# Kernel optimization log

Hardware: AMD Instinct MI355X
Metric: run time of the kernel (lower is better)

## Reference

```python
import jax, jax.numpy as jnp
import numpy as np

INPUTS_SIZE = 128
HIDDEN_SIZE = 256
BATCH = 65536


def hard_sigmoid(x):
    # torch.nn.Hardsigmoid: relu6(x + 3) / 6
    return jnp.clip(x / 6.0 + 0.5, 0.0, 1.0)


def hard_tanh(x):
    return jnp.clip(x, -1.0, 1.0)


def setup_inputs() -> dict:
    key = jax.random.key(0)
    ks = jax.random.split(key, 8)
    cat = INPUTS_SIZE + HIDDEN_SIZE
    s = 1.0 / np.sqrt(cat)
    return {
        "inputs": jax.random.normal(ks[0], (BATCH, INPUTS_SIZE), dtype=jnp.float32),
        "h_prev": jax.random.normal(ks[1], (BATCH, HIDDEN_SIZE), dtype=jnp.float32),
        "W_z": jax.random.uniform(ks[2], (HIDDEN_SIZE, cat), jnp.float32, -s, s),
        "b_z": jax.random.uniform(ks[3], (HIDDEN_SIZE,), jnp.float32, -s, s),
        "W_r": jax.random.uniform(ks[4], (HIDDEN_SIZE, cat), jnp.float32, -s, s),
        "b_r": jax.random.uniform(ks[5], (HIDDEN_SIZE,), jnp.float32, -s, s),
        "W_h": jax.random.uniform(ks[6], (HIDDEN_SIZE, cat), jnp.float32, -s, s),
        "b_h": jax.random.uniform(ks[7], (HIDDEN_SIZE,), jnp.float32, -s, s),
    }


def reference(inputs, h_prev, W_z, b_z, W_r, b_r, W_h, b_h):
    # concat(inputs, h_prev) along feature dim: [B, I+H]
    ih = jnp.concatenate([inputs, h_prev], axis=-1)
    # update gate z and reset gate r (HardSigmoid activations)
    z = hard_sigmoid(ih @ W_z.T + b_z)  # [B, H]
    r = hard_sigmoid(ih @ W_r.T + b_r)  # [B, H]
    # candidate: concat(inputs, r * h_prev) -> linear -> HardTanh
    irh = jnp.concatenate([inputs, r * h_prev], axis=-1)
    h_tilde = hard_tanh(irh @ W_h.T + b_h)  # [B, H]
    # h_next = z * h_prev + (1 - z) * h_tilde
    h_next = z * h_prev + (1.0 - z) * h_tilde
    return h_next
```

## Files before the change

### kernel.cpp

```cpp
#include <hip/hip_runtime.h>


#define BATCH 65536
#define ISZ   128
#define HSZ   256
#define CAT   384
#define BM    64
#define NT    512
#define ROWB  768
#define ACT_B (BM * ROWB)
#define CH_B  16384

using half8   = __attribute__((ext_vector_type(8))) _Float16;
using floatx4 = __attribute__((ext_vector_type(4))) float;

typedef unsigned int u32;
typedef __attribute__((address_space(1))) const u32 gu32;
typedef __attribute__((address_space(3))) u32 lu32;

__device__ __forceinline__ void gload16(const void* g, void* l) {
    __builtin_amdgcn_global_load_lds((gu32*)g, (lu32*)l, 16, 0, 0);
}

#define BAR()      __builtin_amdgcn_s_barrier()
#define SCHED0()   __builtin_amdgcn_sched_barrier(0)
#define WAIT_VM2() asm volatile("s_waitcnt vmcnt(2)" ::: "memory")
#define WAIT_VM0() asm volatile("s_waitcnt vmcnt(0)" ::: "memory")
#define WAIT_LG0() asm volatile("s_waitcnt lgkmcnt(0)" ::: "memory")
#define MFMA       __builtin_amdgcn_mfma_f32_16x16x32_f16

__device__ __forceinline__ float hsig(float x) {
    return fminf(fmaxf(x * (1.0f / 6.0f) + 0.5f, 0.0f), 1.0f);
}
__device__ __forceinline__ float htanh(float x) {
    return fminf(fmaxf(x, -1.0f), 1.0f);
}
__device__ __forceinline__ half8 cvt8(float4 v0, float4 v1) {
    half8 h;
    h[0] = (_Float16)v0.x; h[1] = (_Float16)v0.y;
    h[2] = (_Float16)v0.z; h[3] = (_Float16)v0.w;
    h[4] = (_Float16)v1.x; h[5] = (_Float16)v1.y;
    h[6] = (_Float16)v1.z; h[7] = (_Float16)v1.w;
    return h;
}

__global__ __launch_bounds__(256) void prep_weights(
    const float* __restrict__ Wz, const float* __restrict__ Wr,
    const float* __restrict__ Wh, _Float16* __restrict__ ws)
{
    const int m = blockIdx.y;
    const float* src = (m == 0) ? Wz : (m == 1) ? Wr : Wh;
    _Float16* dst = ws + (size_t)m * (HSZ * CAT);
    const int base = (blockIdx.x * 256 + threadIdx.x) * 8;
    float4 v0 = *(const float4*)(src + base);
    float4 v1 = *(const float4*)(src + base + 4);
    *(half8*)(dst + base) = cvt8(v0, v1);
}

__device__ __forceinline__ void issue_chunk(const _Float16* __restrict__ wf,
                                            unsigned char* wbuf, int c,
                                            int w, int lane) {
    const _Float16* src = (c < 24) ? (wf + (c & 1) * (HSZ * CAT))
                                   : (wf + 2 * (HSZ * CAT));
    const int kk = (c < 24) ? (c >> 1) : (c - 24);
    unsigned char* dst = wbuf + (c & 1) * CH_B;
    #pragma unroll
    for (int ii = 0; ii < 2; ++ii) {
        const int i = w * 2 + ii;
        const int n = i * 16 + (lane >> 2);
        const int ss = (lane & 3) ^ ((n >> 1) & 3);
        gload16(src + n * CAT + kk * 32 + ss * 8, dst + i * 1024);
    }
}

__device__ __forceinline__ half8 wread(const unsigned char* buf, int n, int lk) {
    return *(const half8*)(buf + n * 64 + ((lk ^ ((n >> 1) & 3)) << 4));
}

__global__ __launch_bounds__(NT, 4) void gru_kernel(
    const float* __restrict__ x, const float* __restrict__ h_prev,
    const float* __restrict__ b_z, const float* __restrict__ b_r,
    const float* __restrict__ b_h, const _Float16* __restrict__ wf,
    float* __restrict__ out)
{
    __shared__ __align__(16) unsigned char lds[ACT_B + 2 * CH_B];
    unsigned char* const act  = lds;
    unsigned char* const wbuf = lds + ACT_B;

    const int t    = threadIdx.x;
    const int lane = t & 63;
    const int w    = t >> 6;
    const int mg   = w >> 2;
    const int ng   = w & 3;
    const int lr   = lane & 15;
    const int lk   = lane >> 4;
    const int row0 = blockIdx.x * BM;

    issue_chunk(wf, wbuf, 0, w, lane);
    issue_chunk(wf, wbuf, 1, w, lane);

    float bhv[4];
    floatx4 accz[2][4], accr[2][4];
    #pragma unroll
    for (int j = 0; j < 4; ++j) {
        const int col = ng * 64 + j * 16 + lr;
        const float vz = b_z[col];
        const float vr = b_r[col];
        bhv[j] = b_h[col];
        floatx4 tz = {vz, vz, vz, vz};
        floatx4 tr = {vr, vr, vr, vr};
        accz[0][j] = tz; accz[1][j] = tz;
        accr[0][j] = tr; accr[1][j] = tr;
    }

    for (int c = t; c < BM * 16; c += NT) {
        int row = c >> 4, kc = c & 15;
        const float* g = x + (size_t)(row0 + row) * ISZ + kc * 8;
        float4 v0 = *(const float4*)g;
        float4 v1 = *(const float4*)(g + 4);
        *(half8*)(act + row * ROWB + ((kc * 16) ^ ((row & 7) << 4))) = cvt8(v0, v1);
    }
    for (int c = t; c < BM * 32; c += NT) {
        int row = c >> 5, kc = c & 31;
        const float* g = h_prev + (size_t)(row0 + row) * HSZ + kc * 8;
        float4 v0 = *(const float4*)g;
        float4 v1 = *(const float4*)(g + 4);
        *(half8*)(act + row * ROWB + ((256 + kc * 16) ^ ((row & 7) << 4))) = cvt8(v0, v1);
    }
    WAIT_VM0(); WAIT_LG0(); SCHED0();
    BAR();

    const int rowA = mg * 32 + lr;
    const int asw  = (rowA & 7) << 4;

    half8 a0, a1;

    #pragma unroll 1
    for (int kk = 0; kk < 12; ++kk) {
        WAIT_VM2(); SCHED0(); BAR();
        a0 = *(const half8*)(act + rowA * ROWB        + ((kk * 64 + lk * 16) ^ asw));
        a1 = *(const half8*)(act + (rowA + 16) * ROWB + ((kk * 64 + lk * 16) ^ asw));
        __builtin_amdgcn_s_setprio(1);
        #pragma unroll
        for (int j = 0; j < 4; ++j) {
            half8 bf = wread(wbuf, ng * 64 + j * 16 + lr, lk);
            accz[0][j] = MFMA(a0, bf, accz[0][j], 0, 0, 0);
            accz[1][j] = MFMA(a1, bf, accz[1][j], 0, 0, 0);
        }
        __builtin_amdgcn_s_setprio(0);
        WAIT_LG0(); SCHED0(); BAR();
        issue_chunk(wf, wbuf, 2 * kk + 2, w, lane);
        WAIT_VM2(); SCHED0(); BAR();
        __builtin_amdgcn_s_setprio(1);
        #pragma unroll
        for (int j = 0; j < 4; ++j) {
            half8 bf = wread(wbuf + CH_B, ng * 64 + j * 16 + lr, lk);
            accr[0][j] = MFMA(a0, bf, accr[0][j], 0, 0, 0);
            accr[1][j] = MFMA(a1, bf, accr[1][j], 0, 0, 0);
        }
        __builtin_amdgcn_s_setprio(0);
        WAIT_LG0(); SCHED0(); BAR();
        issue_chunk(wf, wbuf, 2 * kk + 3, w, lane);
    }

    #pragma unroll
    for (int f = 0; f < 2; ++f) {
        #pragma unroll
        for (int j = 0; j < 4; ++j) {
            #pragma unroll
            for (int q = 0; q < 4; ++q) {
                const int row = mg * 32 + f * 16 + lk * 4 + q;
                const int col = ng * 64 + j * 16 + lr;
                accz[f][j][q] = hsig(accz[f][j][q]);
                float rr = hsig(accr[f][j][q]);
                _Float16* hp = (_Float16*)(act + row * ROWB +
                                           ((256 + col * 2) ^ ((row & 7) << 4)));
                float hv = (float)hp[0];
                hp[0] = (_Float16)(rr * hv);
            }
        }
    }
    WAIT_LG0();

    floatx4 acch[2][4];
    #pragma unroll
    for (int j = 0; j < 4; ++j) {
        floatx4 th = {bhv[j], bhv[j], bhv[j], bhv[j]};
        acch[0][j] = th; acch[1][j] = th;
    }
    #pragma unroll 1
    for (int kk = 0; kk < 12; ++kk) {
        if (kk < 11) { WAIT_VM2(); } else { WAIT_VM0(); }
        SCHED0(); BAR();
        const unsigned char* buf = wbuf + (kk & 1) * CH_B;
        a0 = *(const half8*)(act + rowA * ROWB        + ((kk * 64 + lk * 16) ^ asw));
        a1 = *(const half8*)(act + (rowA + 16) * ROWB + ((kk * 64 + lk * 16) ^ asw));
        __builtin_amdgcn_s_setprio(1);
        #pragma unroll
        for (int j = 0; j < 4; ++j) {
            half8 bf = wread(buf, ng * 64 + j * 16 + lr, lk);
            acch[0][j] = MFMA(a0, bf, acch[0][j], 0, 0, 0);
            acch[1][j] = MFMA(a1, bf, acch[1][j], 0, 0, 0);
        }
        __builtin_amdgcn_s_setprio(0);
        WAIT_LG0(); SCHED0(); BAR();
        if (kk < 10) issue_chunk(wf, wbuf, 26 + kk, w, lane);
    }

    #pragma unroll
    for (int f = 0; f < 2; ++f) {
        #pragma unroll
        for (int j = 0; j < 4; ++j) {
            #pragma unroll
            for (int q = 0; q < 4; ++q) {
                const int row = mg * 32 + f * 16 + lk * 4 + q;
                const int col = ng * 64 + j * 16 + lr;
                float ht = htanh(acch[f][j][q]);
                float zz = accz[f][j][q];
                float hv = h_prev[(size_t)(row0 + row) * HSZ + col];
                out[(size_t)(row0 + row) * HSZ + col] = zz * hv + (1.0f - zz) * ht;
            }
        }
    }
}

extern "C" void kernel_launch(void* const* d_in, const int* in_sizes, int n_in,
                              void* d_out, int out_size, void* d_ws, size_t ws_size,
                              hipStream_t stream) {
    const float* x  = (const float*)d_in[0];
    const float* h  = (const float*)d_in[1];
    const float* Wz = (const float*)d_in[2];
    const float* bz = (const float*)d_in[3];
    const float* Wr = (const float*)d_in[4];
    const float* br = (const float*)d_in[5];
    const float* Wh = (const float*)d_in[6];
    const float* bh = (const float*)d_in[7];
    _Float16* wf = (_Float16*)d_ws;

    prep_weights<<<dim3(48, 3), 256, 0, stream>>>(Wz, Wr, Wh, wf);
    gru_kernel<<<dim3(BATCH / BM), NT, 0, stream>>>(
        x, h, bz, br, bh, wf, (float*)d_out);
}
```

Baseline: 198.5 us.

## Halve block to four waves each computing full 64-row tiles per column slice

Cuts the block from eight waves to four. Each wave now covers all 64 rows for a 64-column slice, so every B-fragment read from LDS feeds four MFMAs instead of two, and each wave issues twice as many weight loads per chunk. The r*h_prev product now reads h_prev in fp32 from global memory instead of the fp16 copy in LDS, which slightly changes rounding. The cost is twice the accumulator registers per thread (launch bounds lowered to 2 blocks) and fewer waves to hide latency.

Result: slower. 205.7 us (+3.6%).

```diff
diff --git a/kernel.cpp b/kernel.cpp
--- a/kernel.cpp
+++ b/kernel.cpp
@@ -6,7 +6,7 @@
 #define HSZ   256
 #define CAT   384
 #define BM    64
-#define NT    512
+#define NT    256
 #define ROWB  768
 #define ACT_B (BM * ROWB)
 #define CH_B  16384
@@ -24,7 +24,7 @@
 
 #define BAR()      __builtin_amdgcn_s_barrier()
 #define SCHED0()   __builtin_amdgcn_sched_barrier(0)
-#define WAIT_VM2() asm volatile("s_waitcnt vmcnt(2)" ::: "memory")
+#define WAIT_VM4() asm volatile("s_waitcnt vmcnt(4)" ::: "memory")
 #define WAIT_VM0() asm volatile("s_waitcnt vmcnt(0)" ::: "memory")
 #define WAIT_LG0() asm volatile("s_waitcnt lgkmcnt(0)" ::: "memory")
 #define MFMA       __builtin_amdgcn_mfma_f32_16x16x32_f16
@@ -65,8 +65,8 @@
     const int kk = (c < 24) ? (c >> 1) : (c - 24);
     unsigned char* dst = wbuf + (c & 1) * CH_B;
     #pragma unroll
-    for (int ii = 0; ii < 2; ++ii) {
-        const int i = w * 2 + ii;
+    for (int ii = 0; ii < 4; ++ii) {
+        const int i = w * 4 + ii;
         const int n = i * 16 + (lane >> 2);
         const int ss = (lane & 3) ^ ((n >> 1) & 3);
         gload16(src + n * CAT + kk * 32 + ss * 8, dst + i * 1024);
@@ -77,7 +77,7 @@
     return *(const half8*)(buf + n * 64 + ((lk ^ ((n >> 1) & 3)) << 4));
 }
 
-__global__ __launch_bounds__(NT, 4) void gru_kernel(
+__global__ __launch_bounds__(NT, 2) void gru_kernel(
     const float* __restrict__ x, const float* __restrict__ h_prev,
     const float* __restrict__ b_z, const float* __restrict__ b_r,
     const float* __restrict__ b_h, const _Float16* __restrict__ wf,
@@ -90,8 +90,6 @@
     const int t    = threadIdx.x;
     const int lane = t & 63;
     const int w    = t >> 6;
-    const int mg   = w >> 2;
-    const int ng   = w & 3;
     const int lr   = lane & 15;
     const int lk   = lane >> 4;
     const int row0 = blockIdx.x * BM;
@@ -100,17 +98,17 @@
     issue_chunk(wf, wbuf, 1, w, lane);
 
     float bhv[4];
-    floatx4 accz[2][4], accr[2][4];
+    floatx4 accz[4][4], accr[4][4];
     #pragma unroll
     for (int j = 0; j < 4; ++j) {
-        const int col = ng * 64 + j * 16 + lr;
+        const int col = w * 64 + j * 16 + lr;
         const float vz = b_z[col];
         const float vr = b_r[col];
         bhv[j] = b_h[col];
         floatx4 tz = {vz, vz, vz, vz};
         floatx4 tr = {vr, vr, vr, vr};
-        accz[0][j] = tz; accz[1][j] = tz;
-        accr[0][j] = tr; accr[1][j] = tr;
+        #pragma unroll
+        for (int f = 0; f < 4; ++f) { accz[f][j] = tz; accr[f][j] = tr; }
     }
 
     for (int c = t; c < BM * 16; c += NT) {
@@ -130,33 +128,36 @@
     WAIT_VM0(); WAIT_LG0(); SCHED0();
     BAR();
 
-    const int rowA = mg * 32 + lr;
-    const int asw  = (rowA & 7) << 4;
-
-    half8 a0, a1;
+    half8 a[4];
 
     #pragma unroll 1
     for (int kk = 0; kk < 12; ++kk) {
-        WAIT_VM2(); SCHED0(); BAR();
-        a0 = *(const half8*)(act + rowA * ROWB        + ((kk * 64 + lk * 16) ^ asw));
-        a1 = *(const half8*)(act + (rowA + 16) * ROWB + ((kk * 64 + lk * 16) ^ asw));
+        WAIT_VM4(); SCHED0(); BAR();
+        #pragma unroll
+        for (int f = 0; f < 4; ++f) {
+            const int row = f * 16 + lr;
+            a[f] = *(const half8*)(act + row * ROWB +
+                                   ((kk * 64 + lk * 16) ^ ((row & 7) << 4)));
+        }
         __builtin_amdgcn_s_setprio(1);
         #pragma unroll
         for (int j = 0; j < 4; ++j) {
-            half8 bf = wread(wbuf, ng * 64 + j * 16 + lr, lk);
-            accz[0][j] = MFMA(a0, bf, accz[0][j], 0, 0, 0);
-            accz[1][j] = MFMA(a1, bf, accz[1][j], 0, 0, 0);
+            half8 bf = wread(wbuf, w * 64 + j * 16 + lr, lk);
+            #pragma unroll
+            for (int f = 0; f < 4; ++f)
+                accz[f][j] = MFMA(a[f], bf, accz[f][j], 0, 0, 0);
         }
         __builtin_amdgcn_s_setprio(0);
         WAIT_LG0(); SCHED0(); BAR();
         issue_chunk(wf, wbuf, 2 * kk + 2, w, lane);
-        WAIT_VM2(); SCHED0(); BAR();
+        WAIT_VM4(); SCHED0(); BAR();
         __builtin_amdgcn_s_setprio(1);
         #pragma unroll
         for (int j = 0; j < 4; ++j) {
-            half8 bf = wread(wbuf + CH_B, ng * 64 + j * 16 + lr, lk);
-            accr[0][j] = MFMA(a0, bf, accr[0][j], 0, 0, 0);
-            accr[1][j] = MFMA(a1, bf, accr[1][j], 0, 0, 0);
+            half8 bf = wread(wbuf + CH_B, w * 64 + j * 16 + lr, lk);
+            #pragma unroll
+            for (int f = 0; f < 4; ++f)
+                accr[f][j] = MFMA(a[f], bf, accr[f][j], 0, 0, 0);
         }
         __builtin_amdgcn_s_setprio(0);
         WAIT_LG0(); SCHED0(); BAR();
@@ -164,43 +165,49 @@
     }
 
     #pragma unroll
-    for (int f = 0; f < 2; ++f) {
+    for (int f = 0; f < 4; ++f) {
         #pragma unroll
         for (int j = 0; j < 4; ++j) {
             #pragma unroll
             for (int q = 0; q < 4; ++q) {
-                const int row = mg * 32 + f * 16 + lk * 4 + q;
-                const int col = ng * 64 + j * 16 + lr;
+                const int row = f * 16 + lk * 4 + q;
+                const int col = w * 64 + j * 16 + lr;
                 accz[f][j][q] = hsig(accz[f][j][q]);
                 float rr = hsig(accr[f][j][q]);
-                _Float16* hp = (_Float16*)(act + row * ROWB +
-                                           ((256 + col * 2) ^ ((row & 7) << 4)));
-                float hv = (float)hp[0];
-                hp[0] = (_Float16)(rr * hv);
+                float hv = h_prev[(size_t)(row0 + row) * HSZ + col];
+                *(_Float16*)(act + row * ROWB +
+                             ((256 + col * 2) ^ ((row & 7) << 4))) =
+                    (_Float16)(rr * hv);
             }
         }
     }
     WAIT_LG0();
 
-    floatx4 acch[2][4];
+    floatx4 acch[4][4];
     #pragma unroll
     for (int j = 0; j < 4; ++j) {
         floatx4 th = {bhv[j], bhv[j], bhv[j], bhv[j]};
-        acch[0][j] = th; acch[1][j] = th;
+        #pragma unroll
+        for (int f = 0; f < 4; ++f) acch[f][j] = th;
     }
     #pragma unroll 1
     for (int kk = 0; kk < 12; ++kk) {
-        if (kk < 11) { WAIT_VM2(); } else { WAIT_VM0(); }
+        if (kk < 11) { WAIT_VM4(); } else { WAIT_VM0(); }
         SCHED0(); BAR();
         const unsigned char* buf = wbuf + (kk & 1) * CH_B;
-        a0 = *(const half8*)(act + rowA * ROWB        + ((kk * 64 + lk * 16) ^ asw));
-        a1 = *(const half8*)(act + (rowA + 16) * ROWB + ((kk * 64 + lk * 16) ^ asw));
+        #pragma unroll
+        for (int f = 0; f < 4; ++f) {
+            const int row = f * 16 + lr;
+            a[f] = *(const half8*)(act + row * ROWB +
+                                   ((kk * 64 + lk * 16) ^ ((row & 7) << 4)));
+        }
         __builtin_amdgcn_s_setprio(1);
         #pragma unroll
         for (int j = 0; j < 4; ++j) {
-            half8 bf = wread(buf, ng * 64 + j * 16 + lr, lk);
-            acch[0][j] = MFMA(a0, bf, acch[0][j], 0, 0, 0);
-            acch[1][j] = MFMA(a1, bf, acch[1][j], 0, 0, 0);
+            half8 bf = wread(buf, w * 64 + j * 16 + lr, lk);
+            #pragma unroll
+            for (int f = 0; f < 4; ++f)
+                acch[f][j] = MFMA(a[f], bf, acch[f][j], 0, 0, 0);
         }
         __builtin_amdgcn_s_setprio(0);
         WAIT_LG0(); SCHED0(); BAR();
@@ -208,13 +215,13 @@
     }
 
     #pragma unroll
-    for (int f = 0; f < 2; ++f) {
+    for (int f = 0; f < 4; ++f) {
         #pragma unroll
         for (int j = 0; j < 4; ++j) {
             #pragma unroll
             for (int q = 0; q < 4; ++q) {
-                const int row = mg * 32 + f * 16 + lk * 4 + q;
-                const int col = ng * 64 + j * 16 + lr;
+                const int row = f * 16 + lk * 4 + q;
+                const int col = w * 64 + j * 16 + lr;
                 float ht = htanh(acch[f][j][q]);
                 float zz = accz[f][j][q];
                 float hv = h_prev[(size_t)(row0 + row) * HSZ + col];
```

## Triple-buffer weight chunks and stream x directly from global into registers

Applied to the files above, without the earlier changes.

The weight staging ring grows from two to three LDS buffers. This lets each chunk prefetch be issued before the MFMAs on the current buffer, and removes one barrier per half-iteration. The x portion of the activation tile is no longer staged in LDS. Each wave loads its x fragment from global memory, converts it to fp16 at use during the first four K steps, and re-reads it in the candidate pass. This trades LDS footprint and x staging for extra global loads, and the vmcnt-based waits now have to account for the mixed x and weight loads in flight.

New measurement: 215.5 us. 1.09x slower.

```diff
diff --git a/kernel.cpp b/kernel.cpp
--- a/kernel.cpp
+++ b/kernel.cpp
@@ -7,8 +7,8 @@
 #define CAT   384
 #define BM    64
 #define NT    512
-#define ROWB  768
-#define ACT_B (BM * ROWB)
+#define HROWB 512
+#define ACT_B (BM * HROWB)
 #define CH_B  16384
 
 using half8   = __attribute__((ext_vector_type(8))) _Float16;
@@ -63,7 +63,7 @@
     const _Float16* src = (c < 24) ? (wf + (c & 1) * (HSZ * CAT))
                                    : (wf + 2 * (HSZ * CAT));
     const int kk = (c < 24) ? (c >> 1) : (c - 24);
-    unsigned char* dst = wbuf + (c & 1) * CH_B;
+    unsigned char* dst = wbuf + (c % 3) * CH_B;
     #pragma unroll
     for (int ii = 0; ii < 2; ++ii) {
         const int i = w * 2 + ii;
@@ -83,7 +83,7 @@
     const float* __restrict__ b_h, const _Float16* __restrict__ wf,
     float* __restrict__ out)
 {
-    __shared__ __align__(16) unsigned char lds[ACT_B + 2 * CH_B];
+    __shared__ __align__(16) unsigned char lds[ACT_B + 3 * CH_B];
     unsigned char* const act  = lds;
     unsigned char* const wbuf = lds + ACT_B;
 
@@ -113,56 +113,62 @@
         accr[0][j] = tr; accr[1][j] = tr;
     }
 
-    for (int c = t; c < BM * 16; c += NT) {
-        int row = c >> 4, kc = c & 15;
-        const float* g = x + (size_t)(row0 + row) * ISZ + kc * 8;
-        float4 v0 = *(const float4*)g;
-        float4 v1 = *(const float4*)(g + 4);
-        *(half8*)(act + row * ROWB + ((kc * 16) ^ ((row & 7) << 4))) = cvt8(v0, v1);
-    }
     for (int c = t; c < BM * 32; c += NT) {
         int row = c >> 5, kc = c & 31;
         const float* g = h_prev + (size_t)(row0 + row) * HSZ + kc * 8;
         float4 v0 = *(const float4*)g;
         float4 v1 = *(const float4*)(g + 4);
-        *(half8*)(act + row * ROWB + ((256 + kc * 16) ^ ((row & 7) << 4))) = cvt8(v0, v1);
-    }
-    WAIT_VM0(); WAIT_LG0(); SCHED0();
+        *(half8*)(act + row * HROWB + ((kc * 16) ^ ((row & 7) << 4))) = cvt8(v0, v1);
+    }
+    WAIT_LG0(); SCHED0();
     BAR();
 
     const int rowA = mg * 32 + lr;
-    const int asw  = (rowA & 7) << 4;
+    const int asw  = (lr & 7) << 4;
 
     half8 a0, a1;
 
     #pragma unroll 1
     for (int kk = 0; kk < 12; ++kk) {
         WAIT_VM2(); SCHED0(); BAR();
-        a0 = *(const half8*)(act + rowA * ROWB        + ((kk * 64 + lk * 16) ^ asw));
-        a1 = *(const half8*)(act + (rowA + 16) * ROWB + ((kk * 64 + lk * 16) ^ asw));
+        if (kk < 4) {
+            const float* g0 = x + (size_t)(row0 + rowA) * ISZ + kk * 32 + lk * 8;
+            float4 u0 = *(const float4*)g0;
+            float4 u1 = *(const float4*)(g0 + 4);
+            float4 u2 = *(const float4*)(g0 + 16 * ISZ);
+            float4 u3 = *(const float4*)(g0 + 16 * ISZ + 4);
+            issue_chunk(wf, wbuf, 2 * kk + 2, w, lane);
+            a0 = cvt8(u0, u1);
+            a1 = cvt8(u2, u3);
+        } else {
+            issue_chunk(wf, wbuf, 2 * kk + 2, w, lane);
+            const int off = (kk - 4) * 64 + lk * 16;
+            a0 = *(const half8*)(act + rowA * HROWB        + (off ^ asw));
+            a1 = *(const half8*)(act + (rowA + 16) * HROWB + (off ^ asw));
+        }
+        const unsigned char* bz = wbuf + ((2 * kk) % 3) * CH_B;
         __builtin_amdgcn_s_setprio(1);
         #pragma unroll
         for (int j = 0; j < 4; ++j) {
-            half8 bf = wread(wbuf, ng * 64 + j * 16 + lr, lk);
+            half8 bf = wread(bz, ng * 64 + j * 16 + lr, lk);
             accz[0][j] = MFMA(a0, bf, accz[0][j], 0, 0, 0);
             accz[1][j] = MFMA(a1, bf, accz[1][j], 0, 0, 0);
         }
         __builtin_amdgcn_s_setprio(0);
-        WAIT_LG0(); SCHED0(); BAR();
-        issue_chunk(wf, wbuf, 2 * kk + 2, w, lane);
         WAIT_VM2(); SCHED0(); BAR();
+        issue_chunk(wf, wbuf, 2 * kk + 3, w, lane);
+        const unsigned char* brb = wbuf + ((2 * kk + 1) % 3) * CH_B;
         __builtin_amdgcn_s_setprio(1);
         #pragma unroll
         for (int j = 0; j < 4; ++j) {
-            half8 bf = wread(wbuf + CH_B, ng * 64 + j * 16 + lr, lk);
+            half8 bf = wread(brb, ng * 64 + j * 16 + lr, lk);
             accr[0][j] = MFMA(a0, bf, accr[0][j], 0, 0, 0);
             accr[1][j] = MFMA(a1, bf, accr[1][j], 0, 0, 0);
         }
         __builtin_amdgcn_s_setprio(0);
-        WAIT_LG0(); SCHED0(); BAR();
-        issue_chunk(wf, wbuf, 2 * kk + 3, w, lane);
-    }
-
+    }
+
+    BAR();
     #pragma unroll
     for (int f = 0; f < 2; ++f) {
         #pragma unroll
@@ -173,14 +179,14 @@
                 const int col = ng * 64 + j * 16 + lr;
                 accz[f][j][q] = hsig(accz[f][j][q]);
                 float rr = hsig(accr[f][j][q]);
-                _Float16* hp = (_Float16*)(act + row * ROWB +
-                                           ((256 + col * 2) ^ ((row & 7) << 4)));
+                _Float16* hp = (_Float16*)(act + row * HROWB +
+                                           ((col * 2) ^ ((row & 7) << 4)));
                 float hv = (float)hp[0];
                 hp[0] = (_Float16)(rr * hv);
             }
         }
     }
-    WAIT_LG0();
+    WAIT_LG0(); SCHED0();
 
     floatx4 acch[2][4];
     #pragma unroll
@@ -192,19 +198,30 @@
     for (int kk = 0; kk < 12; ++kk) {
         if (kk < 11) { WAIT_VM2(); } else { WAIT_VM0(); }
         SCHED0(); BAR();
-        const unsigned char* buf = wbuf + (kk & 1) * CH_B;
-        a0 = *(const half8*)(act + rowA * ROWB        + ((kk * 64 + lk * 16) ^ asw));
-        a1 = *(const half8*)(act + (rowA + 16) * ROWB + ((kk * 64 + lk * 16) ^ asw));
+        if (kk < 4) {
+            const float* g0 = x + (size_t)(row0 + rowA) * ISZ + kk * 32 + lk * 8;
+            float4 u0 = *(const float4*)g0;
+            float4 u1 = *(const float4*)(g0 + 4);
+            float4 u2 = *(const float4*)(g0 + 16 * ISZ);
+            float4 u3 = *(const float4*)(g0 + 16 * ISZ + 4);
+            if (kk < 10) issue_chunk(wf, wbuf, 26 + kk, w, lane);
+            a0 = cvt8(u0, u1);
+            a1 = cvt8(u2, u3);
+        } else {
+            if (kk < 10) issue_chunk(wf, wbuf, 26 + kk, w, lane);
+            const int off = (kk - 4) * 64 + lk * 16;
+            a0 = *(const half8*)(act + rowA * HROWB        + (off ^ asw));
+            a1 = *(const half8*)(act + (rowA + 16) * HROWB + (off ^ asw));
+        }
+        const unsigned char* bh_ = wbuf + ((24 + kk) % 3) * CH_B;
         __builtin_amdgcn_s_setprio(1);
         #pragma unroll
         for (int j = 0; j < 4; ++j) {
-            half8 bf = wread(buf, ng * 64 + j * 16 + lr, lk);
+            half8 bf = wread(bh_, ng * 64 + j * 16 + lr, lk);
             acch[0][j] = MFMA(a0, bf, acch[0][j], 0, 0, 0);
             acch[1][j] = MFMA(a1, bf, acch[1][j], 0, 0, 0);
         }
         __builtin_amdgcn_s_setprio(0);
-        WAIT_LG0(); SCHED0(); BAR();
-        if (kk < 10) issue_chunk(wf, wbuf, 26 + kk, w, lane);
     }
 
     #pragma unroll
```

## Load weight fragments directly from global memory in MFMA-ready layout, dropping LDS staging

Applied to the files above, without the earlier changes.

Weights are now converted once into a fragment-ordered fp16 layout, so each lane reads its B operand for the MFMA straight from global memory (L2/cache) and the weights no longer pass through LDS. This removes the double-buffered LDS weight staging and most of the per-step barriers. With less LDS per block the occupancy hint is raised from 4 to 6. In exchange every wave re-reads the weights from cache with no reuse across waves, so the MFMA inputs now carry global-load latency.

Result: slower. 325.9 us (+64.2%).

```diff
diff --git a/kernel.cpp b/kernel.cpp
--- a/kernel.cpp
+++ b/kernel.cpp
@@ -9,25 +9,12 @@
 #define NT    512
 #define ROWB  768
 #define ACT_B (BM * ROWB)
-#define CH_B  16384
+#define MSTR  196608
 
 using half8   = __attribute__((ext_vector_type(8))) _Float16;
 using floatx4 = __attribute__((ext_vector_type(4))) float;
 
-typedef unsigned int u32;
-typedef __attribute__((address_space(1))) const u32 gu32;
-typedef __attribute__((address_space(3))) u32 lu32;
-
-__device__ __forceinline__ void gload16(const void* g, void* l) {
-    __builtin_amdgcn_global_load_lds((gu32*)g, (lu32*)l, 16, 0, 0);
-}
-
-#define BAR()      __builtin_amdgcn_s_barrier()
-#define SCHED0()   __builtin_amdgcn_sched_barrier(0)
-#define WAIT_VM2() asm volatile("s_waitcnt vmcnt(2)" ::: "memory")
-#define WAIT_VM0() asm volatile("s_waitcnt vmcnt(0)" ::: "memory")
-#define WAIT_LG0() asm volatile("s_waitcnt lgkmcnt(0)" ::: "memory")
-#define MFMA       __builtin_amdgcn_mfma_f32_16x16x32_f16
+#define MFMA __builtin_amdgcn_mfma_f32_16x16x32_f16
 
 __device__ __forceinline__ float hsig(float x) {
     return fminf(fmaxf(x * (1.0f / 6.0f) + 0.5f, 0.0f), 1.0f);
@@ -46,46 +33,32 @@
 
 __global__ __launch_bounds__(256) void prep_weights(
     const float* __restrict__ Wz, const float* __restrict__ Wr,
-    const float* __restrict__ Wh, _Float16* __restrict__ ws)
+    const float* __restrict__ Wh, unsigned char* __restrict__ ws)
 {
-    const int m = blockIdx.y;
+    const int m  = blockIdx.y;
+    const int kk = blockIdx.x;
     const float* src = (m == 0) ? Wz : (m == 1) ? Wr : Wh;
-    _Float16* dst = ws + (size_t)m * (HSZ * CAT);
-    const int base = (blockIdx.x * 256 + threadIdx.x) * 8;
-    float4 v0 = *(const float4*)(src + base);
-    float4 v1 = *(const float4*)(src + base + 4);
-    *(half8*)(dst + base) = cvt8(v0, v1);
-}
-
-__device__ __forceinline__ void issue_chunk(const _Float16* __restrict__ wf,
-                                            unsigned char* wbuf, int c,
-                                            int w, int lane) {
-    const _Float16* src = (c < 24) ? (wf + (c & 1) * (HSZ * CAT))
-                                   : (wf + 2 * (HSZ * CAT));
-    const int kk = (c < 24) ? (c >> 1) : (c - 24);
-    unsigned char* dst = wbuf + (c & 1) * CH_B;
-    #pragma unroll
-    for (int ii = 0; ii < 2; ++ii) {
-        const int i = w * 2 + ii;
-        const int n = i * 16 + (lane >> 2);
-        const int ss = (lane & 3) ^ ((n >> 1) & 3);
-        gload16(src + n * CAT + kk * 32 + ss * 8, dst + i * 1024);
-    }
-}
-
-__device__ __forceinline__ half8 wread(const unsigned char* buf, int n, int lk) {
-    return *(const half8*)(buf + n * 64 + ((lk ^ ((n >> 1) & 3)) << 4));
-}
-
-__global__ __launch_bounds__(NT, 4) void gru_kernel(
+    const int t = threadIdx.x;
+    const int l = t & 63;
+    #pragma unroll
+    for (int c4 = 0; c4 < 4; ++c4) {
+        const int c   = c4 * 4 + (t >> 6);
+        const int col = c * 16 + (l & 15);
+        const int k0  = kk * 32 + (l >> 4) * 8;
+        float4 v0 = *(const float4*)(src + col * CAT + k0);
+        float4 v1 = *(const float4*)(src + col * CAT + k0 + 4);
+        *(half8*)(ws + (size_t)(m * 192 + kk * 16 + c) * 1024 + l * 16) =
+            cvt8(v0, v1);
+    }
+}
+
+__global__ __launch_bounds__(NT, 6) void gru_kernel(
     const float* __restrict__ x, const float* __restrict__ h_prev,
     const float* __restrict__ b_z, const float* __restrict__ b_r,
-    const float* __restrict__ b_h, const _Float16* __restrict__ wf,
+    const float* __restrict__ b_h, const unsigned char* __restrict__ wsF,
     float* __restrict__ out)
 {
-    __shared__ __align__(16) unsigned char lds[ACT_B + 2 * CH_B];
-    unsigned char* const act  = lds;
-    unsigned char* const wbuf = lds + ACT_B;
+    __shared__ __align__(16) unsigned char act[ACT_B];
 
     const int t    = threadIdx.x;
     const int lane = t & 63;
@@ -96,8 +69,7 @@
     const int lk   = lane >> 4;
     const int row0 = blockIdx.x * BM;
 
-    issue_chunk(wf, wbuf, 0, w, lane);
-    issue_chunk(wf, wbuf, 1, w, lane);
+    const unsigned char* fb = wsF + (size_t)(ng * 4) * 1024 + lane * 16;
 
     float bhv[4];
     floatx4 accz[2][4], accr[2][4];
@@ -127,41 +99,36 @@
         float4 v1 = *(const float4*)(g + 4);
         *(half8*)(act + row * ROWB + ((256 + kc * 16) ^ ((row & 7) << 4))) = cvt8(v0, v1);
     }
-    WAIT_VM0(); WAIT_LG0(); SCHED0();
-    BAR();
+    __syncthreads();
 
     const int rowA = mg * 32 + lr;
-    const int asw  = (rowA & 7) << 4;
-
-    half8 a0, a1;
-
-    #pragma unroll 1
+    const int asw  = (lr & 7) << 4;
+
+    #pragma unroll 2
     for (int kk = 0; kk < 12; ++kk) {
-        WAIT_VM2(); SCHED0(); BAR();
-        a0 = *(const half8*)(act + rowA * ROWB        + ((kk * 64 + lk * 16) ^ asw));
-        a1 = *(const half8*)(act + (rowA + 16) * ROWB + ((kk * 64 + lk * 16) ^ asw));
-        __builtin_amdgcn_s_setprio(1);
-        #pragma unroll
-        for (int j = 0; j < 4; ++j) {
-            half8 bf = wread(wbuf, ng * 64 + j * 16 + lr, lk);
-            accz[0][j] = MFMA(a0, bf, accz[0][j], 0, 0, 0);
-            accz[1][j] = MFMA(a1, bf, accz[1][j], 0, 0, 0);
-        }
-        __builtin_amdgcn_s_setprio(0);
-        WAIT_LG0(); SCHED0(); BAR();
-        issue_chunk(wf, wbuf, 2 * kk + 2, w, lane);
-        WAIT_VM2(); SCHED0(); BAR();
-        __builtin_amdgcn_s_setprio(1);
-        #pragma unroll
-        for (int j = 0; j < 4; ++j) {
-            half8 bf = wread(wbuf + CH_B, ng * 64 + j * 16 + lr, lk);
-            accr[0][j] = MFMA(a0, bf, accr[0][j], 0, 0, 0);
-            accr[1][j] = MFMA(a1, bf, accr[1][j], 0, 0, 0);
-        }
-        __builtin_amdgcn_s_setprio(0);
-        WAIT_LG0(); SCHED0(); BAR();
-        issue_chunk(wf, wbuf, 2 * kk + 3, w, lane);
-    }
+        half8 a0 = *(const half8*)(act + rowA * ROWB +
+                                   ((kk * 64 + lk * 16) ^ asw));
+        half8 a1 = *(const half8*)(act + (rowA + 16) * ROWB +
+                                   ((kk * 64 + lk * 16) ^ asw));
+        const unsigned char* pk = fb + kk * 16384;
+        half8 bz[4], br[4];
+        #pragma unroll
+        for (int j = 0; j < 4; ++j) bz[j] = *(const half8*)(pk + j * 1024);
+        #pragma unroll
+        for (int j = 0; j < 4; ++j) br[j] = *(const half8*)(pk + MSTR + j * 1024);
+        #pragma unroll
+        for (int j = 0; j < 4; ++j) {
+            accz[0][j] = MFMA(a0, bz[j], accz[0][j], 0, 0, 0);
+            accz[1][j] = MFMA(a1, bz[j], accz[1][j], 0, 0, 0);
+        }
+        #pragma unroll
+        for (int j = 0; j < 4; ++j) {
+            accr[0][j] = MFMA(a0, br[j], accr[0][j], 0, 0, 0);
+            accr[1][j] = MFMA(a1, br[j], accr[1][j], 0, 0, 0);
+        }
+    }
+
+    __syncthreads();
 
     #pragma unroll
     for (int f = 0; f < 2; ++f) {
@@ -180,7 +147,7 @@
             }
         }
     }
-    WAIT_LG0();
+    __syncthreads();
 
     floatx4 acch[2][4];
     #pragma unroll
@@ -188,23 +155,21 @@
         floatx4 th = {bhv[j], bhv[j], bhv[j], bhv[j]};
         acch[0][j] = th; acch[1][j] = th;
     }
-    #pragma unroll 1
+    #pragma unroll 2
     for (int kk = 0; kk < 12; ++kk) {
-        if (kk < 11) { WAIT_VM2(); } else { WAIT_VM0(); }
-        SCHED0(); BAR();
-        const unsigned char* buf = wbuf + (kk & 1) * CH_B;
-        a0 = *(const half8*)(act + rowA * ROWB        + ((kk * 64 + lk * 16) ^ asw));
-        a1 = *(const half8*)(act + (rowA + 16) * ROWB + ((kk * 64 + lk * 16) ^ asw));
-        __builtin_amdgcn_s_setprio(1);
-        #pragma unroll
-        for (int j = 0; j < 4; ++j) {
-            half8 bf = wread(buf, ng * 64 + j * 16 + lr, lk);
-            acch[0][j] = MFMA(a0, bf, acch[0][j], 0, 0, 0);
-            acch[1][j] = MFMA(a1, bf, acch[1][j], 0, 0, 0);
-        }
-        __builtin_amdgcn_s_setprio(0);
-        WAIT_LG0(); SCHED0(); BAR();
-        if (kk < 10) issue_chunk(wf, wbuf, 26 + kk, w, lane);
+        half8 a0 = *(const half8*)(act + rowA * ROWB +
+                                   ((kk * 64 + lk * 16) ^ asw));
+        half8 a1 = *(const half8*)(act + (rowA + 16) * ROWB +
+                                   ((kk * 64 + lk * 16) ^ asw));
+        const unsigned char* pk = fb + 2 * MSTR + kk * 16384;
+        half8 bh[4];
+        #pragma unroll
+        for (int j = 0; j < 4; ++j) bh[j] = *(const half8*)(pk + j * 1024);
+        #pragma unroll
+        for (int j = 0; j < 4; ++j) {
+            acch[0][j] = MFMA(a0, bh[j], acch[0][j], 0, 0, 0);
+            acch[1][j] = MFMA(a1, bh[j], acch[1][j], 0, 0, 0);
+        }
     }
 
     #pragma unroll
@@ -235,9 +200,9 @@
     const float* br = (const float*)d_in[5];
     const float* Wh = (const float*)d_in[6];
     const float* bh = (const float*)d_in[7];
-    _Float16* wf = (_Float16*)d_ws;
-
-    prep_weights<<<dim3(48, 3), 256, 0, stream>>>(Wz, Wr, Wh, wf);
+    unsigned char* wf = (unsigned char*)d_ws;
+
+    prep_weights<<<dim3(12, 3), 256, 0, stream>>>(Wz, Wr, Wh, wf);
     gru_kernel<<<dim3(BATCH / BM), NT, 0, stream>>>(
         x, h, bz, br, bh, wf, (float*)d_out);
 }
```
